# Optimization experiments

Measured on AMD Instinct MI355X. Metric: run time of the kernel, lower is better.

Reference implementation:

```python
import jax, jax.numpy as jnp
import numpy as np


def setup_inputs() -> dict:
    key = jax.random.key(0)
    k1, k2 = jax.random.split(key)
    q, k, d5 = 128, 2048, 768
    return {
        "tgt": jax.random.normal(k1, (q, d5), dtype=jnp.float32),
        "memory": jax.random.normal(k2, (k, d5), dtype=jnp.float32),
        "seq_len": 32,
    }


def reference(tgt, memory, seq_len):
    q, d5 = tgt.shape
    k, _ = memory.shape
    z = d5 // seq_len  # per-token sub-dim
    query_t = tgt.reshape(q, seq_len, z)    # [q, t, d]
    key_m = memory.reshape(k, seq_len, z)   # [k, s, d]
    # Full late-interaction similarity tensor [q, k, s, t]
    score = jnp.einsum('qtd,ksd->qkst', query_t, key_m)
    # max over memory tokens (s) and over query tokens (t), concat, mean
    pooled = jnp.concatenate((score.max(axis=2), score.max(axis=3)), axis=-1)  # [q, k, 2*seq_len]
    score_p = jax.nn.sigmoid(pooled.mean(axis=-1))  # [q, k]
    return (score_p, score_p)
```

## Files before the change

### kernel.cpp

```cpp
#include <hip/hip_runtime.h>
#include <hip/hip_bf16.h>

typedef __bf16 bf16x8 __attribute__((ext_vector_type(8)));
typedef float  f32x16 __attribute__((ext_vector_type(16)));

constexpr int QN  = 128;
constexpr int KN  = 2048;
constexpr int D5  = 768;
constexpr int SL  = 32;
constexpr int ZD  = 24;
constexpr int KCH = 8;

static __device__ __forceinline__ float max3f(float a, float b, float c) {
    return fmaxf(fmaxf(a, b), c);
}

static __device__ __forceinline__ float redmax16(const f32x16& a) {
    float x0 = max3f(a[0],  a[1],  a[2]);
    float x1 = max3f(a[3],  a[4],  a[5]);
    float x2 = max3f(a[6],  a[7],  a[8]);
    float x3 = max3f(a[9],  a[10], a[11]);
    float x4 = max3f(a[12], a[13], a[14]);
    float y0 = max3f(x0, x1, x2);
    float y1 = max3f(x3, x4, a[15]);
    return fmaxf(y0, y1);
}

__global__ __launch_bounds__(256, 8) void matcher_kernel(const float* __restrict__ tgt,
                                                         const float* __restrict__ mem,
                                                         float* __restrict__ out)
{
    __shared__ __align__(16) __bf16 Kf[KCH * 1024];
    __shared__ float vbuf[4][KCH * 32];

    const int tid = threadIdx.x;
    const int kc  = blockIdx.x;
    const int qg  = blockIdx.y;
    const int k0  = kc * KCH;

    {
        const int kl = tid >> 5;
        const int s  = tid & 31;
        const float* src = mem + (size_t)(k0 + kl) * D5 + s * ZD;
        float tv[24];
#pragma unroll
        for (int j = 0; j < 6; ++j) ((float4*)tv)[j] = ((const float4*)src)[j];
        bf16x8 a, b, c, z;
#pragma unroll
        for (int j = 0; j < 8; ++j) {
            a[j] = (__bf16)tv[j];
            b[j] = (__bf16)tv[8 + j];
            c[j] = (__bf16)tv[16 + j];
            z[j] = (__bf16)0.0f;
        }
        __bf16* base = Kf + kl * 1024;
        *(bf16x8*)(base +        s * 8)       = a;
        *(bf16x8*)(base + (32 +  s) * 8)      = b;
        *(bf16x8*)(base + 512 +  s * 8)       = c;
        *(bf16x8*)(base + 512 + (32 + s) * 8) = z;
    }

    const int lane = tid & 63;
    const int wv   = tid >> 6;
    const int t    = lane & 31;
    const int h    = lane >> 5;
    const int q    = qg * 4 + wv;

    const float4* p4 = (const float4*)(tgt + (size_t)q * D5 + t * ZD);
    bf16x8 aQ0, aQ1;
    {
        float4 u0 = p4[2 * h], u1 = p4[2 * h + 1];
        aQ0[0] = (__bf16)u0.x; aQ0[1] = (__bf16)u0.y; aQ0[2] = (__bf16)u0.z; aQ0[3] = (__bf16)u0.w;
        aQ0[4] = (__bf16)u1.x; aQ0[5] = (__bf16)u1.y; aQ0[6] = (__bf16)u1.z; aQ0[7] = (__bf16)u1.w;
        if (h == 0) {
            float4 w0 = p4[4], w1 = p4[5];
            aQ1[0] = (__bf16)w0.x; aQ1[1] = (__bf16)w0.y; aQ1[2] = (__bf16)w0.z; aQ1[3] = (__bf16)w0.w;
            aQ1[4] = (__bf16)w1.x; aQ1[5] = (__bf16)w1.y; aQ1[6] = (__bf16)w1.z; aQ1[7] = (__bf16)w1.w;
        } else {
#pragma unroll
            for (int j = 0; j < 8; ++j) aQ1[j] = (__bf16)0.0f;
        }
    }

    f32x16 zacc;
#pragma unroll
    for (int i = 0; i < 16; ++i) zacc[i] = 0.0f;

    __syncthreads();

    float* vb = vbuf[wv];

#pragma unroll
    for (int kl = 0; kl < KCH; ++kl) {
        const __bf16* lb = Kf + kl * 1024 + lane * 8;
        bf16x8 bK0 = *(const bf16x8*)lb;
        bf16x8 bK1 = *(const bf16x8*)(lb + 512);

        f32x16 accS = __builtin_amdgcn_mfma_f32_32x32x16_bf16(aQ0, bK0, zacc, 0, 0, 0);
        accS        = __builtin_amdgcn_mfma_f32_32x32x16_bf16(aQ1, bK1, accS, 0, 0, 0);
        f32x16 accT = __builtin_amdgcn_mfma_f32_32x32x16_bf16(bK0, aQ0, zacc, 0, 0, 0);
        accT        = __builtin_amdgcn_mfma_f32_32x32x16_bf16(bK1, aQ1, accT, 0, 0, 0);

        float m1 = redmax16(accS);
        float m2 = redmax16(accT);
        m1 = fmaxf(m1, __shfl_xor(m1, 32));
        m2 = fmaxf(m2, __shfl_xor(m2, 32));
        float v = m1 + m2;
        if (h == 0) vb[(kl << 5) + (t ^ kl)] = v;
    }

    {
        const int p = lane & 7;
        const int g = (lane >> 3) & 1;
        float x[16];
#pragma unroll
        for (int i = 0; i < 16; ++i)
            x[i] = vb[(p << 5) + (((g << 4) + i) ^ p)];
        float s0 = (x[0] + x[1]) + (x[2] + x[3]);
        float s1 = (x[4] + x[5]) + (x[6] + x[7]);
        float s2 = (x[8] + x[9]) + (x[10] + x[11]);
        float s3 = (x[12] + x[13]) + (x[14] + x[15]);
        float sum = (s0 + s1) + (s2 + s3);
        sum += __shfl_xor(sum, 8);
        float r = 1.0f / (1.0f + __expf(-sum * (1.0f / 64.0f)));
        if (lane < 8) {
            const int idx = q * KN + k0 + p;
            out[idx] = r;
            out[idx + QN * KN] = r;
        }
    }
}

extern "C" void kernel_launch(void* const* d_in, const int* in_sizes, int n_in,
                              void* d_out, int out_size, void* d_ws, size_t ws_size,
                              hipStream_t stream)
{
    const float* tgt = (const float*)d_in[0];
    const float* mem = (const float*)d_in[1];
    float* out = (float*)d_out;
    dim3 grid(KN / KCH, QN / 4);
    matcher_kernel<<<grid, 256, 0, stream>>>(tgt, mem, out);
}
```

Baseline: 98.42 us.

## Split work per wave as 4 queries by 2 keys and pack max pairs

Each wave now covers 4 queries by 2 keys instead of 1 query by 8 keys. The K fragments are loaded once into registers and the query fragments for all 4 queries are kept in registers, which cuts repeated LDS reads. The cross-half shuffle reductions are replaced by writing both half-wave maxima to LDS as a packed pair of truncated bf16 values, then combining them in the final reduction. Launch bounds are loosened so the larger register footprint fits. The cost is lower occupancy, 4x more global query loads per wave, and extra rounding from truncating the max values to bf16.

New measurement: 101.3 us. 1.03x slower.

```diff
diff --git a/kernel.cpp b/kernel.cpp
--- a/kernel.cpp
+++ b/kernel.cpp
@@ -3,11 +3,11 @@
 
 typedef __bf16 bf16x8 __attribute__((ext_vector_type(8)));
 typedef float  f32x16 __attribute__((ext_vector_type(16)));
+typedef unsigned int u32;
 
 constexpr int QN  = 128;
 constexpr int KN  = 2048;
 constexpr int D5  = 768;
-constexpr int SL  = 32;
 constexpr int ZD  = 24;
 constexpr int KCH = 8;
 
@@ -26,12 +26,12 @@
     return fmaxf(y0, y1);
 }
 
-__global__ __launch_bounds__(256, 8) void matcher_kernel(const float* __restrict__ tgt,
+__global__ __launch_bounds__(256, 3) void matcher_kernel(const float* __restrict__ tgt,
                                                          const float* __restrict__ mem,
                                                          float* __restrict__ out)
 {
     __shared__ __align__(16) __bf16 Kf[KCH * 1024];
-    __shared__ float vbuf[4][KCH * 32];
+    __shared__ __align__(16) u32 vbuf[4 * 512];
 
     const int tid = threadIdx.x;
     const int kc  = blockIdx.x;
@@ -64,21 +64,26 @@
     const int wv   = tid >> 6;
     const int t    = lane & 31;
     const int h    = lane >> 5;
-    const int q    = qg * 4 + wv;
 
-    const float4* p4 = (const float4*)(tgt + (size_t)q * D5 + t * ZD);
-    bf16x8 aQ0, aQ1;
-    {
+    bf16x8 aQ0[4], aQ1[4];
+#pragma unroll
+    for (int qq = 0; qq < 4; ++qq) {
+        const int q = qg * 4 + qq;
+        const float4* p4 = (const float4*)(tgt + (size_t)q * D5 + t * ZD);
         float4 u0 = p4[2 * h], u1 = p4[2 * h + 1];
-        aQ0[0] = (__bf16)u0.x; aQ0[1] = (__bf16)u0.y; aQ0[2] = (__bf16)u0.z; aQ0[3] = (__bf16)u0.w;
-        aQ0[4] = (__bf16)u1.x; aQ0[5] = (__bf16)u1.y; aQ0[6] = (__bf16)u1.z; aQ0[7] = (__bf16)u1.w;
+        aQ0[qq][0] = (__bf16)u0.x; aQ0[qq][1] = (__bf16)u0.y;
+        aQ0[qq][2] = (__bf16)u0.z; aQ0[qq][3] = (__bf16)u0.w;
+        aQ0[qq][4] = (__bf16)u1.x; aQ0[qq][5] = (__bf16)u1.y;
+        aQ0[qq][6] = (__bf16)u1.z; aQ0[qq][7] = (__bf16)u1.w;
         if (h == 0) {
             float4 w0 = p4[4], w1 = p4[5];
-            aQ1[0] = (__bf16)w0.x; aQ1[1] = (__bf16)w0.y; aQ1[2] = (__bf16)w0.z; aQ1[3] = (__bf16)w0.w;
-            aQ1[4] = (__bf16)w1.x; aQ1[5] = (__bf16)w1.y; aQ1[6] = (__bf16)w1.z; aQ1[7] = (__bf16)w1.w;
+            aQ1[qq][0] = (__bf16)w0.x; aQ1[qq][1] = (__bf16)w0.y;
+            aQ1[qq][2] = (__bf16)w0.z; aQ1[qq][3] = (__bf16)w0.w;
+            aQ1[qq][4] = (__bf16)w1.x; aQ1[qq][5] = (__bf16)w1.y;
+            aQ1[qq][6] = (__bf16)w1.z; aQ1[qq][7] = (__bf16)w1.w;
         } else {
 #pragma unroll
-            for (int j = 0; j < 8; ++j) aQ1[j] = (__bf16)0.0f;
+            for (int j = 0; j < 8; ++j) aQ1[qq][j] = (__bf16)0.0f;
         }
     }
 
@@ -88,43 +93,56 @@
 
     __syncthreads();
 
-    float* vb = vbuf[wv];
+    bf16x8 bK0[2], bK1[2];
+#pragma unroll
+    for (int j = 0; j < 2; ++j) {
+        const __bf16* base = Kf + (wv * 2 + j) * 1024 + lane * 8;
+        bK0[j] = *(const bf16x8*)base;
+        bK1[j] = *(const bf16x8*)(base + 512);
+    }
+
+    u32* vbw = vbuf + wv * 512;
+    const int cbase = h * 32;
 
 #pragma unroll
-    for (int kl = 0; kl < KCH; ++kl) {
-        const __bf16* lb = Kf + kl * 1024 + lane * 8;
-        bf16x8 bK0 = *(const bf16x8*)lb;
-        bf16x8 bK1 = *(const bf16x8*)(lb + 512);
-
-        f32x16 accS = __builtin_amdgcn_mfma_f32_32x32x16_bf16(aQ0, bK0, zacc, 0, 0, 0);
-        accS        = __builtin_amdgcn_mfma_f32_32x32x16_bf16(aQ1, bK1, accS, 0, 0, 0);
-        f32x16 accT = __builtin_amdgcn_mfma_f32_32x32x16_bf16(bK0, aQ0, zacc, 0, 0, 0);
-        accT        = __builtin_amdgcn_mfma_f32_32x32x16_bf16(bK1, aQ1, accT, 0, 0, 0);
+    for (int p = 0; p < 8; ++p) {
+        const int qq = p >> 1, j = p & 1;
+        f32x16 accS = __builtin_amdgcn_mfma_f32_32x32x16_bf16(aQ0[qq], bK0[j], zacc, 0, 0, 0);
+        accS        = __builtin_amdgcn_mfma_f32_32x32x16_bf16(aQ1[qq], bK1[j], accS, 0, 0, 0);
+        f32x16 accT = __builtin_amdgcn_mfma_f32_32x32x16_bf16(bK0[j], aQ0[qq], zacc, 0, 0, 0);
+        accT        = __builtin_amdgcn_mfma_f32_32x32x16_bf16(bK1[j], aQ1[qq], accT, 0, 0, 0);
 
         float m1 = redmax16(accS);
         float m2 = redmax16(accT);
-        m1 = fmaxf(m1, __shfl_xor(m1, 32));
-        m2 = fmaxf(m2, __shfl_xor(m2, 32));
-        float v = m1 + m2;
-        if (h == 0) vb[(kl << 5) + (t ^ kl)] = v;
+        u32 pk = (__float_as_uint(m1) & 0xFFFF0000u) | (__float_as_uint(m2) >> 16);
+        vbw[p * 64 + cbase + (t ^ ((4 * p) & 31))] = pk;
     }
 
     {
-        const int p = lane & 7;
-        const int g = (lane >> 3) & 1;
-        float x[16];
+        const int p = lane >> 3;
+        const int e = lane & 7;
+        const u32* g = vbw + p * 64 + ((4 * e) ^ ((4 * p) & 31));
+        uint4 g0 = *(const uint4*)g;
+        uint4 g1 = *(const uint4*)(g + 32);
+        u32 w0[4] = {g0.x, g0.y, g0.z, g0.w};
+        u32 w1[4] = {g1.x, g1.y, g1.z, g1.w};
+        float sum = 0.0f;
 #pragma unroll
-        for (int i = 0; i < 16; ++i)
-            x[i] = vb[(p << 5) + (((g << 4) + i) ^ p)];
-        float s0 = (x[0] + x[1]) + (x[2] + x[3]);
-        float s1 = (x[4] + x[5]) + (x[6] + x[7]);
-        float s2 = (x[8] + x[9]) + (x[10] + x[11]);
-        float s3 = (x[12] + x[13]) + (x[14] + x[15]);
-        float sum = (s0 + s1) + (s2 + s3);
-        sum += __shfl_xor(sum, 8);
+        for (int i = 0; i < 4; ++i) {
+            float a1 = __uint_as_float(w0[i] & 0xFFFF0000u);
+            float a2 = __uint_as_float(w0[i] << 16);
+            float b1 = __uint_as_float(w1[i] & 0xFFFF0000u);
+            float b2 = __uint_as_float(w1[i] << 16);
+            sum += fmaxf(a1, b1) + fmaxf(a2, b2);
+        }
+        sum += __shfl_xor(sum, 1);
+        sum += __shfl_xor(sum, 2);
+        sum += __shfl_xor(sum, 4);
         float r = 1.0f / (1.0f + __expf(-sum * (1.0f / 64.0f)));
-        if (lane < 8) {
-            const int idx = q * KN + k0 + p;
+        if (e == 0) {
+            const int q  = qg * 4 + (p >> 1);
+            const int kk = k0 + wv * 2 + (p & 1);
+            const int idx = q * KN + kk;
             out[idx] = r;
             out[idx + QN * KN] = r;
         }
```
